# Kernel tuning notes

Measured on AMD Instinct MI355X. Metric: run time of the kernel, lower is better.

The kernel has to match this reference:

```python
import jax, jax.numpy as jnp
import numpy as np
import math

B, S, D, H = 2, 2048, 1024, 16
HD = D // H  # head dim = 64


def setup_inputs() -> dict:
    key = jax.random.key(0)
    ks = jax.random.split(key, 8)
    scale = 1.0 / math.sqrt(D)
    return {
        "x": jax.random.normal(ks[0], (B, S, D), dtype=jnp.float32),
        "mask": jax.random.randint(ks[1], (B, S, S), 0, 2).astype(bool),
        "Wq": jax.random.normal(ks[2], (D, D), dtype=jnp.float32) * scale,
        "bq": jax.random.normal(ks[3], (D,), dtype=jnp.float32) * 0.01,
        "Wk": jax.random.normal(ks[4], (D, D), dtype=jnp.float32) * scale,
        "bk": jax.random.normal(ks[5], (D,), dtype=jnp.float32) * 0.01,
        "Wv": jax.random.normal(ks[6], (D, D), dtype=jnp.float32) * scale,
        "bv": jax.random.normal(ks[7], (D,), dtype=jnp.float32) * 0.01,
    }


def reference(x, mask, Wq, bq, Wk, bk, Wv, bv):
    # Linear projections (weights stored as [in, out])
    q = x @ Wq + bq  # [B,S,D]
    k = x @ Wk + bk
    v = x @ Wv + bv
    # split heads -> [B,H,S,HD]
    q = q.reshape(B, S, H, HD).transpose(0, 2, 1, 3)
    k = k.reshape(B, S, H, HD).transpose(0, 2, 1, 3)
    v = v.reshape(B, S, H, HD).transpose(0, 2, 1, 3)
    scores = jnp.einsum("bhqd,bhkd->bhqk", q, k) / jnp.sqrt(jnp.float32(HD))
    # Faithful to the source: masked_fill_(mask, -inf) is immediately
    # overwritten by masked_fill_(mask, 0), so masked positions end up 0
    # BEFORE the softmax (a quirk of the original module).
    scores = jnp.where(mask[:, None, :, :], 0.0, scores)
    attn = jax.nn.softmax(scores, axis=-1)  # dropout=0.0 (eval)
    out = jnp.einsum("bhqk,bhkd->bhqd", attn, v)
    return out.transpose(0, 2, 1, 3).reshape(B, S, D)
```

## Files before the change

### kernel.cpp

```cpp
#include <hip/hip_runtime.h>
#include <cstdint>
#include <cstddef>

static constexpr int B_ = 2, S_ = 2048, D_ = 1024, H_ = 16, HD_ = 64;

typedef float f32x4 __attribute__((ext_vector_type(4)));
typedef short bf16x8 __attribute__((ext_vector_type(8)));

__device__ __forceinline__ unsigned short f2bf(float f) {
    union { float f; unsigned int u; } v; v.f = f;
    unsigned int r = v.u + 0x7FFFu + ((v.u >> 16) & 1u);
    return (unsigned short)(r >> 16);
}

__device__ __forceinline__ unsigned pack2bf(float a, float b) {
#if __has_builtin(__builtin_amdgcn_cvt_pk_bf16_f32)
    auto p = __builtin_amdgcn_cvt_pk_bf16_f32(a, b);
    unsigned u; __builtin_memcpy(&u, &p, 4);
    return u;
#else
    return (unsigned)f2bf(a) | ((unsigned)f2bf(b) << 16);
#endif
}

__device__ __forceinline__ void gload_lds16(const void* g, void* l) {
    __builtin_amdgcn_global_load_lds(
        (const __attribute__((address_space(1))) void*)g,
        (__attribute__((address_space(3))) void*)l, 16, 0, 0);
}

__global__ __launch_bounds__(256)
void prep(const float* __restrict__ x, unsigned short* __restrict__ xo,
          const int* __restrict__ m, unsigned char* __restrict__ mo,
          const float* __restrict__ Wq, const float* __restrict__ Wk,
          const float* __restrict__ Wv, unsigned short* __restrict__ wt) {
    __shared__ unsigned short Ts[64][72];
    const int bid = blockIdx.x, t = threadIdx.x;
    if (bid < 2048) {
        size_t i = ((size_t)bid * 256 + t) * 8;
        float4 a = *(const float4*)(x + i);
        float4 c = *(const float4*)(x + i + 4);
        uint4 r;
        r.x = pack2bf(a.x, a.y); r.y = pack2bf(a.z, a.w);
        r.z = pack2bf(c.x, c.y); r.w = pack2bf(c.z, c.w);
        *(uint4*)(xo + i) = r;
    } else if (bid < 4096) {
        size_t i = ((size_t)(bid - 2048) * 256 + t) * 16;
        uint4 r;
        unsigned w[4];
        #pragma unroll
        for (int g = 0; g < 4; ++g) {
            int4 v = *(const int4*)(m + i + g * 4);
            w[g] = (v.x ? 1u : 0u) | (v.y ? 1u << 8 : 0u) |
                   (v.z ? 1u << 16 : 0u) | (v.w ? 1u << 24 : 0u);
        }
        r.x = w[0]; r.y = w[1]; r.z = w[2]; r.w = w[3];
        *(uint4*)(mo + i) = r;
    } else {
        const int tid = bid - 4096;
        const int mat = tid >> 8, tile = tid & 255;
        const float* __restrict__ W = (mat == 0) ? Wq : (mat == 1) ? Wk : Wv;
        unsigned short* __restrict__ o = wt + (size_t)mat * D_ * D_;
        const int n0 = (tile & 15) * 64, k0 = (tile >> 4) * 64;
        {
            const int nl = t & 63, kb = t >> 6;
            #pragma unroll
            for (int i = 0; i < 16; ++i) {
                int k = kb + i * 4;
                Ts[nl][k] = f2bf(W[(size_t)(k0 + k) * D_ + n0 + nl]);
            }
        }
        __syncthreads();
        {
            const int kl = t & 63, nb = t >> 6;
            #pragma unroll
            for (int i = 0; i < 16; ++i) {
                int n = nb + i * 4;
                o[(size_t)(n0 + n) * D_ + k0 + kl] = Ts[n][kl];
            }
        }
    }
}

__global__ __launch_bounds__(256)
void qkv_gemm(const unsigned short* __restrict__ xb, const unsigned short* __restrict__ wt,
              const float* __restrict__ bq, const float* __restrict__ bk,
              const float* __restrict__ bv,
              unsigned short* __restrict__ qo, unsigned short* __restrict__ ko,
              unsigned short* __restrict__ vto) {
    const int bx = blockIdx.x;
    const int by = blockIdx.y;
    const int mat = bx >> 3;
    const int ncol0 = (bx & 7) * 128;
    const float* __restrict__ bias = (mat == 0) ? bq : (mat == 1) ? bk : bv;
    const unsigned short* __restrict__ Wm = wt + (size_t)mat * D_ * D_;

    __shared__ unsigned short As[2][128 * 32];
    __shared__ unsigned short Bs[2][128 * 32];

    const int t = threadIdx.x;
    const int w = t >> 6, lane = t & 63;
    const int l15 = lane & 15, quad = lane >> 4;
    const int mw = (w >> 1) * 64, nw = (w & 1) * 64;
    const int rowBase = by * 128;

    const int r16 = lane >> 2;
    const int sslot = lane & 3;
    const int sg = (sslot ^ ((r16 >> 1) & 3)) * 8;
    const int rcol = (quad ^ ((l15 >> 1) & 3)) * 8;

    f32x4 acc[4][4] = {};

    #pragma unroll
    for (int j = 0; j < 2; ++j) {
        const int r0 = w * 32 + j * 16;
        gload_lds16(xb + (size_t)(rowBase + r0 + r16) * D_ + sg, &As[0][r0 * 32]);
        gload_lds16(Wm + (size_t)(ncol0 + r0 + r16) * D_ + sg, &Bs[0][r0 * 32]);
    }

    for (int it = 0; it < 32; ++it) {
        const int cur = it & 1;
        __syncthreads();
        if (it + 1 < 32) {
            const int ktn = (it + 1) * 32;
            #pragma unroll
            for (int j = 0; j < 2; ++j) {
                const int r0 = w * 32 + j * 16;
                gload_lds16(xb + (size_t)(rowBase + r0 + r16) * D_ + ktn + sg,
                            &As[cur ^ 1][r0 * 32]);
                gload_lds16(Wm + (size_t)(ncol0 + r0 + r16) * D_ + ktn + sg,
                            &Bs[cur ^ 1][r0 * 32]);
            }
        }

        bf16x8 a[4], b[4];
        #pragma unroll
        for (int i = 0; i < 4; ++i)
            a[i] = *(const bf16x8*)&As[cur][(mw + i * 16 + l15) * 32 + rcol];
        #pragma unroll
        for (int j = 0; j < 4; ++j)
            b[j] = *(const bf16x8*)&Bs[cur][(nw + j * 16 + l15) * 32 + rcol];
        #pragma unroll
        for (int i = 0; i < 4; ++i)
            #pragma unroll
            for (int j = 0; j < 4; ++j)
                acc[i][j] = __builtin_amdgcn_mfma_f32_16x16x32_bf16(a[i], b[j], acc[i][j], 0, 0, 0);
    }

    if (mat < 2) {
        unsigned short* __restrict__ O = (mat == 0) ? qo : ko;
        const float osc = (mat == 0) ? 0.18033688011112443f : 1.0f;
        #pragma unroll
        for (int j = 0; j < 4; ++j) {
            const int col = ncol0 + nw + j * 16 + l15;
            const float bb = bias[col];
            #pragma unroll
            for (int i = 0; i < 4; ++i)
                #pragma unroll
                for (int r = 0; r < 4; ++r) {
                    const int m = rowBase + mw + i * 16 + quad * 4 + r;
                    O[(size_t)m * D_ + col] = f2bf((acc[i][j][r] + bb) * osc);
                }
        }
    } else {
        #pragma unroll
        for (int j = 0; j < 4; ++j) {
            const int col = ncol0 + nw + j * 16 + l15;
            const float bb = bias[col];
            const int hh = col >> 6, hd = col & 63;
            #pragma unroll
            for (int i = 0; i < 4; ++i) {
                const int m0 = rowBase + mw + i * 16 + quad * 4;
                const int bg = m0 >> 11, s0 = m0 & 2047;
                ushort4 pk;
                pk.x = f2bf(acc[i][j][0] + bb);
                pk.y = f2bf(acc[i][j][1] + bb);
                pk.z = f2bf(acc[i][j][2] + bb);
                pk.w = f2bf(acc[i][j][3] + bb);
                *(ushort4*)&vto[(((size_t)bg * H_ + hh) * HD_ + hd) * S_ + s0] = pk;
            }
        }
    }
}

__global__ __launch_bounds__(256)
void attn_mfma(const unsigned short* __restrict__ qmat,
               const unsigned short* __restrict__ kmat,
               const unsigned short* __restrict__ vtg,
               const unsigned char* __restrict__ msk, float* __restrict__ out) {
    const int h = blockIdx.x, qt = blockIdx.y, b = blockIdx.z;
    const int t = threadIdx.x, w = t >> 6, lane = t & 63;
    const int l15 = lane & 15, quad = lane >> 4;
    const int q0 = qt * 128;

    __shared__ unsigned short Ks[2][64 * 64];
    __shared__ unsigned short Vs[2][64 * 64];
    __shared__ __align__(16) unsigned short Ps[128][72];

    const size_t bh = (size_t)b * S_ * D_ + (size_t)h * HD_;
    const unsigned short* __restrict__ qp = qmat + bh;
    const unsigned short* __restrict__ kp = kmat + bh;
    const unsigned short* __restrict__ vp = vtg + ((size_t)b * H_ + h) * HD_ * S_;
    const unsigned char* __restrict__ mb = msk + (size_t)b * S_ * S_;

    const int rs = lane >> 3, sslot = lane & 7;
    const int sg = (sslot ^ rs) * 8;

    bf16x8 qfr[2][2];
    #pragma unroll
    for (int nt = 0; nt < 2; ++nt)
        #pragma unroll
        for (int kst = 0; kst < 2; ++kst)
            qfr[nt][kst] = *(const bf16x8*)(qp +
                (size_t)(q0 + w * 32 + nt * 16 + l15) * D_ + kst * 32 + quad * 8);

    f32x4 accO[2][4] = {};
    f32x4 lsA[2] = {};
    bf16x8 ones;
    #pragma unroll
    for (int i = 0; i < 8; ++i) ones[i] = (short)0x3F80;

    #pragma unroll
    for (int j = 0; j < 2; ++j) {
        const int rb = w * 16 + j * 8;
        gload_lds16(kp + (size_t)(rb + rs) * D_ + sg, &Ks[0][rb * 64]);
        gload_lds16(vp + (size_t)(rb + rs) * S_ + sg, &Vs[0][rb * 64]);
    }

    for (int it = 0; it < 32; ++it) {
        const int cur = it & 1;
        const int kt = it * 64;
        __syncthreads();

        unsigned mu[2][4];
        #pragma unroll
        for (int nt = 0; nt < 2; ++nt) {
            const int qr = w * 32 + nt * 16 + l15;
            const unsigned char* __restrict__ mrow = mb + (size_t)(q0 + qr) * S_ + kt;
            #pragma unroll
            for (int mt = 0; mt < 4; ++mt)
                mu[nt][mt] = *(const unsigned*)(mrow + mt * 16 + quad * 4);
        }

        if (it + 1 < 32) {
            const int ktn = kt + 64;
            #pragma unroll
            for (int j = 0; j < 2; ++j) {
                const int rb = w * 16 + j * 8;
                gload_lds16(kp + (size_t)(ktn + rb + rs) * D_ + sg, &Ks[cur ^ 1][rb * 64]);
                gload_lds16(vp + (size_t)(rb + rs) * S_ + ktn + sg, &Vs[cur ^ 1][rb * 64]);
            }
        }

        f32x4 sc[4][2] = {};
        #pragma unroll
        for (int kst = 0; kst < 2; ++kst) {
            bf16x8 kfr[4];
            #pragma unroll
            for (int mt = 0; mt < 4; ++mt) {
                const int R = mt * 16 + l15;
                kfr[mt] = *(const bf16x8*)&Ks[cur][R * 64 + (((kst * 4 + quad) ^ (l15 & 7)) * 8)];
            }
            #pragma unroll
            for (int mt = 0; mt < 4; ++mt)
                #pragma unroll
                for (int nt = 0; nt < 2; ++nt)
                    sc[mt][nt] = __builtin_amdgcn_mfma_f32_16x16x32_bf16(kfr[mt], qfr[nt][kst], sc[mt][nt], 0, 0, 0);
        }

        #pragma unroll
        for (int nt = 0; nt < 2; ++nt) {
            const int qr = w * 32 + nt * 16 + l15;
            #pragma unroll
            for (int mt = 0; mt < 4; ++mt) {
                float p[4];
                #pragma unroll
                for (int r = 0; r < 4; ++r) {
                    float e = __builtin_amdgcn_exp2f(sc[mt][nt][r]);
                    p[r] = ((mu[nt][mt] >> (8 * r)) & 0xFFu) ? 1.0f : e;
                }
                uint2 pk;
                pk.x = pack2bf(p[0], p[1]);
                pk.y = pack2bf(p[2], p[3]);
                *(uint2*)&Ps[qr][mt * 16 + quad * 4] = pk;
            }
        }

        #pragma unroll
        for (int kst = 0; kst < 2; ++kst) {
            bf16x8 vfr[4];
            #pragma unroll
            for (int dt = 0; dt < 4; ++dt) {
                const int R = dt * 16 + l15;
                vfr[dt] = *(const bf16x8*)&Vs[cur][R * 64 + (((kst * 4 + quad) ^ (l15 & 7)) * 8)];
            }
            #pragma unroll
            for (int mt = 0; mt < 2; ++mt) {
                bf16x8 pfr = *(const bf16x8*)&Ps[w * 32 + mt * 16 + l15][kst * 32 + quad * 8];
                #pragma unroll
                for (int dt = 0; dt < 4; ++dt)
                    accO[mt][dt] = __builtin_amdgcn_mfma_f32_16x16x32_bf16(pfr, vfr[dt], accO[mt][dt], 0, 0, 0);
                lsA[mt] = __builtin_amdgcn_mfma_f32_16x16x32_bf16(pfr, ones, lsA[mt], 0, 0, 0);
            }
        }
    }

    float* __restrict__ ob = out + ((size_t)b * S_ + q0) * D_ + (size_t)h * HD_;
    #pragma unroll
    for (int mt = 0; mt < 2; ++mt)
        #pragma unroll
        for (int r = 0; r < 4; ++r) {
            const float inv = 1.0f / lsA[mt][r];
            const int qr = w * 32 + mt * 16 + quad * 4 + r;
            #pragma unroll
            for (int dt = 0; dt < 4; ++dt)
                ob[(size_t)qr * D_ + dt * 16 + l15] = accO[mt][dt][r] * inv;
        }
}

extern "C" void kernel_launch(void* const* d_in, const int* in_sizes, int n_in,
                              void* d_out, int out_size, void* d_ws, size_t ws_size,
                              hipStream_t stream) {
    (void)in_sizes; (void)n_in; (void)out_size; (void)ws_size;
    const float* x    = (const float*)d_in[0];
    const int*   mask = (const int*)d_in[1];
    const float* Wq   = (const float*)d_in[2];
    const float* bq   = (const float*)d_in[3];
    const float* Wk   = (const float*)d_in[4];
    const float* bk   = (const float*)d_in[5];
    const float* Wv   = (const float*)d_in[6];
    const float* bv   = (const float*)d_in[7];
    float* out = (float*)d_out;

    const size_t M1 = (size_t)1024 * 1024;
    unsigned short* xb  = (unsigned short*)d_ws;
    unsigned short* wtb = xb + 4 * M1;
    unsigned short* qb  = wtb + 3 * M1;
    unsigned short* kb  = qb + 4 * M1;
    unsigned short* vtb = kb + 4 * M1;
    unsigned char*  mk  = (unsigned char*)(vtb + 4 * M1);

    prep<<<4864, 256, 0, stream>>>(x, xb, mask, mk, Wq, Wk, Wv, wtb);
    qkv_gemm<<<dim3(24, 32), 256, 0, stream>>>(xb, wtb, bq, bk, bv, qb, kb, vtb);
    attn_mfma<<<dim3(16, 16, 2), 256, 0, stream>>>(qb, kb, vtb, mk, out);
}
```

Baseline: 235.5 us.

## Halve attention query tile and add branchless mask select with swizzled P buffer

Result: slower. 246.1 us (+4.5%).

```diff
diff --git a/kernel.cpp b/kernel.cpp
--- a/kernel.cpp
+++ b/kernel.cpp
@@ -51,8 +51,8 @@
         #pragma unroll
         for (int g = 0; g < 4; ++g) {
             int4 v = *(const int4*)(m + i + g * 4);
-            w[g] = (v.x ? 1u : 0u) | (v.y ? 1u << 8 : 0u) |
-                   (v.z ? 1u << 16 : 0u) | (v.w ? 1u << 24 : 0u);
+            w[g] = (v.x ? 0xFFu : 0u) | (v.y ? 0xFF00u : 0u) |
+                   (v.z ? 0xFF0000u : 0u) | (v.w ? 0xFF000000u : 0u);
         }
         r.x = w[0]; r.y = w[1]; r.z = w[2]; r.w = w[3];
         *(uint4*)(mo + i) = r;
@@ -183,7 +183,7 @@
     }
 }
 
-__global__ __launch_bounds__(256)
+__global__ __launch_bounds__(256, 4)
 void attn_mfma(const unsigned short* __restrict__ qmat,
                const unsigned short* __restrict__ kmat,
                const unsigned short* __restrict__ vtg,
@@ -191,11 +191,11 @@
     const int h = blockIdx.x, qt = blockIdx.y, b = blockIdx.z;
     const int t = threadIdx.x, w = t >> 6, lane = t & 63;
     const int l15 = lane & 15, quad = lane >> 4;
-    const int q0 = qt * 128;
+    const int q0 = qt * 64;
 
     __shared__ unsigned short Ks[2][64 * 64];
     __shared__ unsigned short Vs[2][64 * 64];
-    __shared__ __align__(16) unsigned short Ps[128][72];
+    __shared__ __align__(16) unsigned short Ps[64 * 64];
 
     const size_t bh = (size_t)b * S_ * D_ + (size_t)h * HD_;
     const unsigned short* __restrict__ qp = qmat + bh;
@@ -206,16 +206,16 @@
     const int rs = lane >> 3, sslot = lane & 7;
     const int sg = (sslot ^ rs) * 8;
 
-    bf16x8 qfr[2][2];
-    #pragma unroll
-    for (int nt = 0; nt < 2; ++nt)
-        #pragma unroll
-        for (int kst = 0; kst < 2; ++kst)
-            qfr[nt][kst] = *(const bf16x8*)(qp +
-                (size_t)(q0 + w * 32 + nt * 16 + l15) * D_ + kst * 32 + quad * 8);
-
-    f32x4 accO[2][4] = {};
-    f32x4 lsA[2] = {};
+    const int qr = w * 16 + l15;
+    const int sw7 = l15 & 7;
+
+    bf16x8 qfr[2];
+    #pragma unroll
+    for (int kst = 0; kst < 2; ++kst)
+        qfr[kst] = *(const bf16x8*)(qp + (size_t)(q0 + qr) * D_ + kst * 32 + quad * 8);
+
+    f32x4 accO[4] = {};
+    f32x4 lsA = {};
     bf16x8 ones;
     #pragma unroll
     for (int i = 0; i < 8; ++i) ones[i] = (short)0x3F80;
@@ -232,14 +232,12 @@
         const int kt = it * 64;
         __syncthreads();
 
-        unsigned mu[2][4];
-        #pragma unroll
-        for (int nt = 0; nt < 2; ++nt) {
-            const int qr = w * 32 + nt * 16 + l15;
+        unsigned mu[4];
+        {
             const unsigned char* __restrict__ mrow = mb + (size_t)(q0 + qr) * S_ + kt;
             #pragma unroll
             for (int mt = 0; mt < 4; ++mt)
-                mu[nt][mt] = *(const unsigned*)(mrow + mt * 16 + quad * 4);
+                mu[mt] = *(const unsigned*)(mrow + mt * 16 + quad * 4);
         }
 
         if (it + 1 < 32) {
@@ -252,38 +250,35 @@
             }
         }
 
-        f32x4 sc[4][2] = {};
+        f32x4 sc[4] = {};
         #pragma unroll
         for (int kst = 0; kst < 2; ++kst) {
             bf16x8 kfr[4];
             #pragma unroll
             for (int mt = 0; mt < 4; ++mt) {
                 const int R = mt * 16 + l15;
-                kfr[mt] = *(const bf16x8*)&Ks[cur][R * 64 + (((kst * 4 + quad) ^ (l15 & 7)) * 8)];
-            }
+                kfr[mt] = *(const bf16x8*)&Ks[cur][R * 64 + (((kst * 4 + quad) ^ sw7) * 8)];
+            }
+            __builtin_amdgcn_s_setprio(1);
             #pragma unroll
             for (int mt = 0; mt < 4; ++mt)
-                #pragma unroll
-                for (int nt = 0; nt < 2; ++nt)
-                    sc[mt][nt] = __builtin_amdgcn_mfma_f32_16x16x32_bf16(kfr[mt], qfr[nt][kst], sc[mt][nt], 0, 0, 0);
-        }
-
-        #pragma unroll
-        for (int nt = 0; nt < 2; ++nt) {
-            const int qr = w * 32 + nt * 16 + l15;
-            #pragma unroll
-            for (int mt = 0; mt < 4; ++mt) {
-                float p[4];
-                #pragma unroll
-                for (int r = 0; r < 4; ++r) {
-                    float e = __builtin_amdgcn_exp2f(sc[mt][nt][r]);
-                    p[r] = ((mu[nt][mt] >> (8 * r)) & 0xFFu) ? 1.0f : e;
-                }
-                uint2 pk;
-                pk.x = pack2bf(p[0], p[1]);
-                pk.y = pack2bf(p[2], p[3]);
-                *(uint2*)&Ps[qr][mt * 16 + quad * 4] = pk;
-            }
+                sc[mt] = __builtin_amdgcn_mfma_f32_16x16x32_bf16(kfr[mt], qfr[kst], sc[mt], 0, 0, 0);
+            __builtin_amdgcn_s_setprio(0);
+        }
+
+        #pragma unroll
+        for (int mt = 0; mt < 4; ++mt) {
+            unsigned p0 = pack2bf(__builtin_amdgcn_exp2f(sc[mt][0]),
+                                  __builtin_amdgcn_exp2f(sc[mt][1]));
+            unsigned p1 = pack2bf(__builtin_amdgcn_exp2f(sc[mt][2]),
+                                  __builtin_amdgcn_exp2f(sc[mt][3]));
+            const unsigned m0 = __builtin_amdgcn_perm(0u, mu[mt], 0x01010000u);
+            const unsigned m1 = __builtin_amdgcn_perm(0u, mu[mt], 0x03030202u);
+            p0 = (m0 & 0x3F803F80u) | (~m0 & p0);
+            p1 = (m1 & 0x3F803F80u) | (~m1 & p1);
+            uint2 pk2; pk2.x = p0; pk2.y = p1;
+            *(uint2*)((char*)Ps + qr * 128 +
+                      (((2 * mt + (quad >> 1)) ^ sw7) * 16) + (quad & 1) * 8) = pk2;
         }
 
         #pragma unroll
@@ -292,30 +287,28 @@
             #pragma unroll
             for (int dt = 0; dt < 4; ++dt) {
                 const int R = dt * 16 + l15;
-                vfr[dt] = *(const bf16x8*)&Vs[cur][R * 64 + (((kst * 4 + quad) ^ (l15 & 7)) * 8)];
-            }
-            #pragma unroll
-            for (int mt = 0; mt < 2; ++mt) {
-                bf16x8 pfr = *(const bf16x8*)&Ps[w * 32 + mt * 16 + l15][kst * 32 + quad * 8];
-                #pragma unroll
-                for (int dt = 0; dt < 4; ++dt)
-                    accO[mt][dt] = __builtin_amdgcn_mfma_f32_16x16x32_bf16(pfr, vfr[dt], accO[mt][dt], 0, 0, 0);
-                lsA[mt] = __builtin_amdgcn_mfma_f32_16x16x32_bf16(pfr, ones, lsA[mt], 0, 0, 0);
-            }
+                vfr[dt] = *(const bf16x8*)&Vs[cur][R * 64 + (((kst * 4 + quad) ^ sw7) * 8)];
+            }
+            bf16x8 pfr = *(const bf16x8*)((const char*)Ps + qr * 128 +
+                                          (((kst * 4 + quad) ^ sw7) * 16));
+            __builtin_amdgcn_s_setprio(1);
+            #pragma unroll
+            for (int dt = 0; dt < 4; ++dt)
+                accO[dt] = __builtin_amdgcn_mfma_f32_16x16x32_bf16(pfr, vfr[dt], accO[dt], 0, 0, 0);
+            lsA = __builtin_amdgcn_mfma_f32_16x16x32_bf16(pfr, ones, lsA, 0, 0, 0);
+            __builtin_amdgcn_s_setprio(0);
         }
     }
 
     float* __restrict__ ob = out + ((size_t)b * S_ + q0) * D_ + (size_t)h * HD_;
     #pragma unroll
-    for (int mt = 0; mt < 2; ++mt)
-        #pragma unroll
-        for (int r = 0; r < 4; ++r) {
-            const float inv = 1.0f / lsA[mt][r];
-            const int qr = w * 32 + mt * 16 + quad * 4 + r;
-            #pragma unroll
-            for (int dt = 0; dt < 4; ++dt)
-                ob[(size_t)qr * D_ + dt * 16 + l15] = accO[mt][dt][r] * inv;
-        }
+    for (int r = 0; r < 4; ++r) {
+        const float inv = 1.0f / lsA[r];
+        const int row = w * 16 + quad * 4 + r;
+        #pragma unroll
+        for (int dt = 0; dt < 4; ++dt)
+            ob[(size_t)row * D_ + dt * 16 + l15] = accO[dt][r] * inv;
+    }
 }
 
 extern "C" void kernel_launch(void* const* d_in, const int* in_sizes, int n_in,
@@ -342,5 +335,5 @@
 
     prep<<<4864, 256, 0, stream>>>(x, xb, mask, mk, Wq, Wk, Wv, wtb);
     qkv_gemm<<<dim3(24, 32), 256, 0, stream>>>(xb, wtb, bq, bk, bv, qb, kb, vtb);
-    attn_mfma<<<dim3(16, 16, 2), 256, 0, stream>>>(qb, kb, vtb, mk, out);
-}
+    attn_mfma<<<dim3(16, 32, 2), 256, 0, stream>>>(qb, kb, vtb, mk, out);
+}
```
